# Kernel optimization log

Measured on AMD Instinct MI355X. Metric: run time of the kernel, lower is better.

## Reference

```python
import jax, jax.numpy as jnp
import numpy as np

THRESHOLD = 1.0  # CIF firing threshold (init kwarg)


def setup_inputs() -> dict:
    key = jax.random.key(0)
    k1, k2 = jax.random.split(key)
    B, T, H = 32, 2048, 512
    return {
        "hidden": jax.random.normal(k1, (B, T, H), dtype=jnp.float32),
        "alphas": jax.random.uniform(k2, (B, T), dtype=jnp.float32),
        "integrate": jnp.zeros((B,), dtype=jnp.float32),
        "frame": jnp.zeros((B, H), dtype=jnp.float32),
    }


def cif_scan(hidden, alphas, integrate, frame, threshold):
    """Continuous integrate-and-fire recurrence over time, vectorized over batch.

    hidden: [B,T,H], alphas: [B,T], integrate: [B], frame: [B,H]
    Returns fires [B,T], frames [B,T,H], integrate_new [B], frame_new [B,H].
    """

    def step(carry, inp):
        integ, fr = carry          # [B], [B,H]
        alpha, h_t = inp           # [B], [B,H]
        dist_completion = 1.0 - integ
        integ = integ + alpha
        fire = integ >= threshold                       # [B] bool
        integ_next = jnp.where(fire, integ - 1.0, integ)
        cur = jnp.where(fire, dist_completion, alpha)   # weight spent this step
        rem = alpha - cur                               # leftover weight after firing
        fr_out = fr + cur[:, None] * h_t                # frame recorded at this step
        fr_next = jnp.where(fire[:, None], rem[:, None] * h_t, fr_out)
        return (integ_next, fr_next), (integ, fr_out)

    xs = (jnp.swapaxes(alphas, 0, 1), jnp.swapaxes(hidden, 0, 1))  # time-major
    (integ_f, frame_f), (fires_t, frames_t) = jax.lax.scan(step, (integrate, frame), xs)
    fires = jnp.swapaxes(fires_t, 0, 1)    # [B,T]
    frames = jnp.swapaxes(frames_t, 0, 1)  # [B,T,H]
    return fires, frames, integ_f, frame_f


def reference(hidden, alphas, integrate, frame):
    T = hidden.shape[1]
    fires, frames, integ_new, frame_new = cif_scan(hidden, alphas, integrate, frame, THRESHOLD)
    # torch.index_select(frames[0], 0, nonzero(fires[0] >= threshold)) -> data-dependent
    # shape; emulate with jit-safe padded nonzero (padding rows replicate row 0).
    idx = jnp.nonzero(fires[0] >= THRESHOLD, size=T, fill_value=0)[0]
    frame_sel = frames[0][idx]  # [T, H], first num_fires rows are the fired frames
    return frame_sel, integ_new, frame_new
```

## Files before the change

### kernel.cpp

```cpp
#include <hip/hip_runtime.h>


#define THRESH 1.0f
#define MAXB   64
#define MAXT   2048
#define MAXCH  (MAXT / 64)
#define SC4    2048

__device__ __forceinline__ float fract_exact(float x) {
    float r; asm("v_fract_f32 %0, %1" : "=v"(r) : "v"(x)); return r;
}

__global__ __launch_bounds__(512, 2) void cif_prep_kernel(
    const float4* __restrict__ a4,
    const float*  __restrict__ integ0,
    float4* __restrict__ aT4,
    float*  __restrict__ gT,
    int* __restrict__ rowStart, int* __restrict__ rowEnd, int* __restrict__ rowFlags,
    int* __restrict__ tlast,
    float* __restrict__ integ_out,
    int B, int T)
{
    const int tid = threadIdx.x;
    const int T4 = T >> 2;
    const int nchunk = T >> 6;

    __shared__ float4             s_abuf0[SC4];
    __shared__ float4             s_abuf1[SC4];
    __shared__ float              s_ci[MAXCH * MAXB];
    __shared__ unsigned long long s_mask[MAXCH * MAXB];
    __shared__ int                s_fire[MAXT];
    __shared__ int                s_nf, s_f0;

    for (int i = tid; i < B * T4; i += 512) {
        const int b = i / T4, c = i - b * T4;
        aT4[(size_t)c * B + b] = a4[i];
    }
    __syncthreads();

    const int SPS = (SC4 * 4) / B;
    const int NSC = T / SPS;
    const int cpsc = SPS >> 6;

    for (int i = tid; i < SC4; i += 512) s_abuf0[i] = aT4[i];
    __syncthreads();

    float integ = (tid < B) ? integ0[tid] : 0.0f;

    for (int sc = 0; sc < NSC; ++sc) {
        if (tid >= 64) {
            if (sc + 1 < NSC) {
                const float4* src = aT4 + (size_t)(sc + 1) * SC4;
                float4* dst = (sc & 1) ? s_abuf0 : s_abuf1;
                for (int i = tid - 64; i < SC4; i += 448) dst[i] = src[i];
            }
        } else if (tid < B) {
            const float4* sb = (sc & 1) ? s_abuf1 : s_abuf0;
            const int cbase = sc * cpsc;
            for (int cl = 0; cl < cpsc; ++cl) {
                s_ci[(cbase + cl) * B + tid] = integ;
                float4 rb[16];
#pragma unroll
                for (int j = 0; j < 16; ++j)
                    rb[j] = sb[(cl * 16 + j) * B + tid];
                __builtin_amdgcn_sched_barrier(0);
#pragma unroll
                for (int j = 0; j < 16; ++j) {
                    integ = fract_exact(integ + rb[j].x);
                    integ = fract_exact(integ + rb[j].y);
                    integ = fract_exact(integ + rb[j].z);
                    integ = fract_exact(integ + rb[j].w);
                }
            }
        }
        __syncthreads();
    }
    if (tid < B) integ_out[tid] = integ;

    for (int w = tid; w < nchunk * B; w += 512) {
        const int c = w / B, b = w - c * B;
        float ig = s_ci[w];
        unsigned long long m = 0;
        for (int j = 0; j < 16; ++j) {
            const float4 av4 = aT4[(size_t)(c * 16 + j) * B + b];
            const float av[4] = {av4.x, av4.y, av4.z, av4.w};
            float gv[4];
#pragma unroll
            for (int k = 0; k < 4; ++k) {
                const int idx = j * 4 + k;
                const float alpha = av[k];
                const float s   = ig + alpha;
                const bool fire = (s >= THRESH);
                const float sm1 = s - 1.0f;
                ig = fire ? sm1 : s;
                gv[k] = fire ? sm1 : alpha;
                m |= fire ? (1ull << idx) : 0ull;
            }
#pragma unroll
            for (int k = 0; k < 4; ++k)
                gT[(size_t)(c * 64 + j * 4 + k) * B + b] = gv[k];
        }
        s_mask[w] = m;
    }
    __syncthreads();

    if (tid < B) {
        int tl = -1;
        for (int c = nchunk - 1; c >= 0; --c) {
            const unsigned long long mc = s_mask[c * B + tid];
            if (mc) { tl = c * 64 + 63 - __clzll(mc); break; }
        }
        tlast[tid] = tl;
    }
    if (tid < 64) {
        unsigned long long m0 = (tid < nchunk) ? s_mask[tid * B] : 0ull;
        const int pc = __popcll(m0);
        int x = pc;
#pragma unroll
        for (int d = 1; d < 64; d <<= 1) {
            const int y = __shfl_up(x, d);
            if (tid >= d) x += y;
        }
        if (tid == 63) s_nf = x;
        if (tid == 0)  s_f0 = (int)(m0 & 1ull);
        int r = x - pc;
        while (m0) {
            const int p = __ffsll(m0) - 1;
            s_fire[r++] = tid * 64 + p;
            m0 &= m0 - 1;
        }
    }
    __syncthreads();

    const int nf = s_nf, f0 = s_f0;
    for (int r = tid; r < T; r += 512) {
        int st, en, fl;
        if (r < nf) {
            en = s_fire[r];
            st = (r == 0) ? 0 : s_fire[r - 1];
            fl = ((r == 0) ? 1 : 0) | 2;
        } else {
            st = 0; en = 0; fl = 1 | (f0 ? 2 : 0);
        }
        rowStart[r] = st; rowEnd[r] = en; rowFlags[r] = fl;
    }
}

__global__ __launch_bounds__(128) void cif_out_kernel(
    const float* __restrict__ hidden,
    const float* __restrict__ frame0,
    const float* __restrict__ gT,
    const float* __restrict__ alphas,
    const int* __restrict__ rowStart, const int* __restrict__ rowEnd,
    const int* __restrict__ rowFlags, const int* __restrict__ tlast,
    float* __restrict__ out_sel,
    float* __restrict__ frame_out,
    int B, int T, int H)
{
    const int blk = blockIdx.x;

    if (blk < T) {
        const int r = blk;
        const int start = rowStart[r], end = rowEnd[r], fl = rowFlags[r];
        const float a  = alphas[end];
        const float ge = gT[(size_t)end * B];
        const float wend = (fl & 2) ? (a - ge) : a;
        for (int h0 = threadIdx.x * 4; h0 < H; h0 += 128 * 4) {
            float4 acc = (fl & 1) ? *reinterpret_cast<const float4*>(frame0 + h0)
                                  : make_float4(0.f, 0.f, 0.f, 0.f);
            for (int s = start; s < end; ++s) {
                const float  w  = gT[(size_t)s * B];
                const float4 hv = *reinterpret_cast<const float4*>(hidden + (size_t)s * H + h0);
                acc.x += w * hv.x; acc.y += w * hv.y;
                acc.z += w * hv.z; acc.w += w * hv.w;
            }
            const float4 hv = *reinterpret_cast<const float4*>(hidden + (size_t)end * H + h0);
            acc.x += wend * hv.x; acc.y += wend * hv.y;
            acc.z += wend * hv.z; acc.w += wend * hv.w;
            *reinterpret_cast<float4*>(out_sel + (size_t)r * H + h0) = acc;
        }
    } else {
        const int b  = blk - T;
        const int tl = tlast[b];
        const int start = (tl < 0) ? 0 : tl;
        const float* hb = hidden + (size_t)b * T * H;
        for (int h0 = threadIdx.x * 4; h0 < H; h0 += 128 * 4) {
            float4 acc = (tl < 0) ? *reinterpret_cast<const float4*>(frame0 + (size_t)b * H + h0)
                                  : make_float4(0.f, 0.f, 0.f, 0.f);
            for (int s = start; s < T; ++s) {
                const float  w  = gT[(size_t)s * B + b];
                const float4 hv = *reinterpret_cast<const float4*>(hb + (size_t)s * H + h0);
                acc.x += w * hv.x; acc.y += w * hv.y;
                acc.z += w * hv.z; acc.w += w * hv.w;
            }
            *reinterpret_cast<float4*>(frame_out + (size_t)b * H + h0) = acc;
        }
    }
}

extern "C" void kernel_launch(void* const* d_in, const int* in_sizes, int n_in,
                              void* d_out, int out_size, void* d_ws, size_t ws_size,
                              hipStream_t stream) {
    const float* hidden    = (const float*)d_in[0];
    const float* alphas    = (const float*)d_in[1];
    const float* integrate = (const float*)d_in[2];
    const float* frame     = (const float*)d_in[3];

    const int B = in_sizes[2];
    const int T = in_sizes[1] / B;
    const int H = in_sizes[3] / B;

    float* out       = (float*)d_out;
    float* out_sel   = out;
    float* integ_out = out + (size_t)T * H;
    float* frame_out = integ_out + B;

    char* ws = (char*)d_ws;
    float4* aT4   = (float4*)ws;  ws += sizeof(float) * (size_t)B * T;
    float*  gT    = (float*)ws;   ws += sizeof(float) * (size_t)B * T;
    int* rowStart = (int*)ws;     ws += sizeof(int) * T;
    int* rowEnd   = (int*)ws;     ws += sizeof(int) * T;
    int* rowFlags = (int*)ws;     ws += sizeof(int) * T;
    int* tlast    = (int*)ws;     ws += sizeof(int) * B;

    cif_prep_kernel<<<1, 512, 0, stream>>>(
        (const float4*)alphas, integrate, aT4, gT,
        rowStart, rowEnd, rowFlags, tlast, integ_out, B, T);

    cif_out_kernel<<<T + B, 128, 0, stream>>>(
        hidden, frame, gT, alphas, rowStart, rowEnd, rowFlags, tlast,
        out_sel, frame_out, B, T, H);
}
```

Before: 227.7 us.

## Drop global alpha transpose; transpose into LDS while staging, keep gT batch-major

The single-block prep kernel no longer writes a time-major copy of alphas to global memory and then reads it back. Each superchunk is read straight from the batch-major alphas and transposed while being stored into the shared-memory double buffer. The gate array gT becomes batch-major and is written as float4, so the output kernel reads per-batch weights contiguously. This removes a serial global round trip from a one-block kernel, at the cost of strided gathers during staging.

```diff
diff --git a/kernel.cpp b/kernel.cpp
--- a/kernel.cpp
+++ b/kernel.cpp
@@ -12,9 +12,9 @@
 }
 
 __global__ __launch_bounds__(512, 2) void cif_prep_kernel(
-    const float4* __restrict__ a4,
+    const float4* __restrict__ a4g,
+    const float*  __restrict__ alphas,
     const float*  __restrict__ integ0,
-    float4* __restrict__ aT4,
     float*  __restrict__ gT,
     int* __restrict__ rowStart, int* __restrict__ rowEnd, int* __restrict__ rowFlags,
     int* __restrict__ tlast,
@@ -32,17 +32,16 @@
     __shared__ int                s_fire[MAXT];
     __shared__ int                s_nf, s_f0;
 
-    for (int i = tid; i < B * T4; i += 512) {
-        const int b = i / T4, c = i - b * T4;
-        aT4[(size_t)c * B + b] = a4[i];
-    }
-    __syncthreads();
-
-    const int SPS = (SC4 * 4) / B;
+    const int G  = SC4;
+    const int GP = G / B;
+    const int SPS = GP * 4;
     const int NSC = T / SPS;
     const int cpsc = SPS >> 6;
 
-    for (int i = tid; i < SC4; i += 512) s_abuf0[i] = aT4[i];
+    for (int i = tid; i < G; i += 512) {
+        const int b = i / GP, t4l = i - b * GP;
+        s_abuf0[t4l * B + b] = a4g[b * T4 + t4l];
+    }
     __syncthreads();
 
     float integ = (tid < B) ? integ0[tid] : 0.0f;
@@ -50,9 +49,12 @@
     for (int sc = 0; sc < NSC; ++sc) {
         if (tid >= 64) {
             if (sc + 1 < NSC) {
-                const float4* src = aT4 + (size_t)(sc + 1) * SC4;
                 float4* dst = (sc & 1) ? s_abuf0 : s_abuf1;
-                for (int i = tid - 64; i < SC4; i += 448) dst[i] = src[i];
+                const int t4base = (sc + 1) * GP;
+                for (int i = tid - 64; i < G; i += 448) {
+                    const int b = i / GP, t4l = i - b * GP;
+                    dst[t4l * B + b] = a4g[b * T4 + t4base + t4l];
+                }
             }
         } else if (tid < B) {
             const float4* sb = (sc & 1) ? s_abuf1 : s_abuf0;
@@ -77,12 +79,13 @@
     }
     if (tid < B) integ_out[tid] = integ;
 
+    float4* gT4 = (float4*)gT;
     for (int w = tid; w < nchunk * B; w += 512) {
-        const int c = w / B, b = w - c * B;
-        float ig = s_ci[w];
+        const int b = w / nchunk, c = w - b * nchunk;
+        float ig = s_ci[c * B + b];
         unsigned long long m = 0;
         for (int j = 0; j < 16; ++j) {
-            const float4 av4 = aT4[(size_t)(c * 16 + j) * B + b];
+            const float4 av4 = a4g[b * T4 + c * 16 + j];
             const float av[4] = {av4.x, av4.y, av4.z, av4.w};
             float gv[4];
 #pragma unroll
@@ -96,11 +99,9 @@
                 gv[k] = fire ? sm1 : alpha;
                 m |= fire ? (1ull << idx) : 0ull;
             }
-#pragma unroll
-            for (int k = 0; k < 4; ++k)
-                gT[(size_t)(c * 64 + j * 4 + k) * B + b] = gv[k];
-        }
-        s_mask[w] = m;
+            gT4[b * T4 + c * 16 + j] = make_float4(gv[0], gv[1], gv[2], gv[3]);
+        }
+        s_mask[c * B + b] = m;
     }
     __syncthreads();
 
@@ -163,13 +164,13 @@
         const int r = blk;
         const int start = rowStart[r], end = rowEnd[r], fl = rowFlags[r];
         const float a  = alphas[end];
-        const float ge = gT[(size_t)end * B];
+        const float ge = gT[end];
         const float wend = (fl & 2) ? (a - ge) : a;
         for (int h0 = threadIdx.x * 4; h0 < H; h0 += 128 * 4) {
             float4 acc = (fl & 1) ? *reinterpret_cast<const float4*>(frame0 + h0)
                                   : make_float4(0.f, 0.f, 0.f, 0.f);
             for (int s = start; s < end; ++s) {
-                const float  w  = gT[(size_t)s * B];
+                const float  w  = gT[s];
                 const float4 hv = *reinterpret_cast<const float4*>(hidden + (size_t)s * H + h0);
                 acc.x += w * hv.x; acc.y += w * hv.y;
                 acc.z += w * hv.z; acc.w += w * hv.w;
@@ -184,11 +185,12 @@
         const int tl = tlast[b];
         const int start = (tl < 0) ? 0 : tl;
         const float* hb = hidden + (size_t)b * T * H;
+        const float* gb = gT + (size_t)b * T;
         for (int h0 = threadIdx.x * 4; h0 < H; h0 += 128 * 4) {
             float4 acc = (tl < 0) ? *reinterpret_cast<const float4*>(frame0 + (size_t)b * H + h0)
                                   : make_float4(0.f, 0.f, 0.f, 0.f);
             for (int s = start; s < T; ++s) {
-                const float  w  = gT[(size_t)s * B + b];
+                const float  w  = gb[s];
                 const float4 hv = *reinterpret_cast<const float4*>(hb + (size_t)s * H + h0);
                 acc.x += w * hv.x; acc.y += w * hv.y;
                 acc.z += w * hv.z; acc.w += w * hv.w;
@@ -216,7 +218,6 @@
     float* frame_out = integ_out + B;
 
     char* ws = (char*)d_ws;
-    float4* aT4   = (float4*)ws;  ws += sizeof(float) * (size_t)B * T;
     float*  gT    = (float*)ws;   ws += sizeof(float) * (size_t)B * T;
     int* rowStart = (int*)ws;     ws += sizeof(int) * T;
     int* rowEnd   = (int*)ws;     ws += sizeof(int) * T;
@@ -224,7 +225,7 @@
     int* tlast    = (int*)ws;     ws += sizeof(int) * B;
 
     cif_prep_kernel<<<1, 512, 0, stream>>>(
-        (const float4*)alphas, integrate, aT4, gT,
+        (const float4*)alphas, alphas, integrate, gT,
         rowStart, rowEnd, rowFlags, tlast, integ_out, B, T);
 
     cif_out_kernel<<<T + B, 128, 0, stream>>>(
```

Measured after the change: 212.9 us. 1.07x faster.
